# Kernel tuning notes

Measured on AMD Instinct MI355X. Metric: run time of the kernel, lower is better.

## Reference

```python
import jax, jax.numpy as jnp
import numpy as np

DIM = 96          # dense volume side (N_VOX / 2**(n_layer-scale-1) with scale=2)
C = 24            # ch_in[scale]
FEAT_INIT = 0.0   # not direct_substitute


def _scatter_channel(coords, values, ch, default, dtype=jnp.float32):
    """sparse_to_dense_channel: dense[x,y,z] = values; OOB coords are dropped."""
    vol = jnp.full((DIM, DIM, DIM, ch), default, dtype=dtype)
    return vol.at[coords[:, 0], coords[:, 1], coords[:, 2]].set(values, mode='drop')


def _mask_coords(coords, valid):
    # Replace invalid rows with an out-of-bounds index so scatter mode='drop' skips them
    return jnp.where(valid[:, None], coords, DIM)


def setup_inputs() -> dict:
    key = jax.random.key(0)
    ks = jax.random.split(key, 9)
    return {
        'current_coords': jax.random.randint(ks[0], (150000, 3), 0, DIM, dtype=jnp.int32),
        'current_values': jax.random.normal(ks[1], (150000, C), dtype=jnp.float32),
        'global_coords_raw': jax.random.randint(ks[2], (200000, 3), 0, 160, dtype=jnp.int32),
        'global_values': jax.random.normal(ks[3], (200000, C), dtype=jnp.float32),
        'coords_target_global': jax.random.randint(ks[4], (100000, 3), 0, DIM, dtype=jnp.int32),
        'tsdf_target': jax.random.uniform(ks[5], (100000,), dtype=jnp.float32) * 2.0 - 1.0,
        'global_coords_target_raw': jax.random.randint(ks[6], (120000, 3), 0, 160, dtype=jnp.int32),
        'global_tsdf_target': jax.random.uniform(ks[7], (120000, 1), dtype=jnp.float32) * 2.0 - 1.0,
        'relative_origin': jax.random.randint(ks[8], (3,), 0, 32, dtype=jnp.int32),
    }


def reference(current_coords, current_values, global_coords_raw, global_values,
              coords_target_global, tsdf_target, global_coords_target_raw,
              global_tsdf_target, relative_origin):
    # --- shift global coords into current fragment frame, compute FBV mask ---
    gc = global_coords_raw - relative_origin[None, :]
    valid = jnp.all((gc >= 0) & (gc < DIM), axis=-1)                     # (M,)

    # --- FUSION.FULL is False: keep only global voxels present in current sparse set ---
    valid_volume = jnp.zeros((DIM, DIM, DIM), dtype=jnp.int32)
    valid_volume = valid_volume.at[current_coords[:, 0], current_coords[:, 1],
                                   current_coords[:, 2]].set(1, mode='drop')
    gcc = jnp.clip(gc, 0, DIM - 1)
    occ = valid_volume[gcc[:, 0], gcc[:, 1], gcc[:, 2]]
    valid = valid & (occ != 0)

    # --- dense scatters (sparse_to_dense_channel) ---
    global_volume = _scatter_channel(_mask_coords(gc, valid), global_values, C, FEAT_INIT)
    current_volume = _scatter_channel(current_coords, current_values, C, FEAT_INIT)

    # updated_coords = current_coords (FULL is False branch)
    updated_coords = current_coords

    gtc = global_coords_target_raw - relative_origin[None, :]
    valid_target = jnp.all((gtc >= 0) & (gtc < DIM), axis=-1)            # (Mt,)
    coords_target = jnp.concatenate([_mask_coords(gtc, valid_target), coords_target_global], axis=0)
    tsdf_all = jnp.concatenate([global_tsdf_target, tsdf_target[:, None]], axis=0)
    target_volume = _scatter_channel(coords_target, tsdf_all, 1, 1.0)

    return updated_coords, current_volume, global_volume, target_volume, valid, valid_target
```

## Files before the change

### kernel.cpp

```cpp
#include <hip/hip_runtime.h>

#define DIMV 96
#define NCH 24
constexpr int VOX = DIMV * DIMV * DIMV;
constexpr int N_CUR = 150000;
constexpr int N_GLB = 200000;
constexpr int N_TGT_LOC = 100000;
constexpr int N_TGT_GLB = 120000;

constexpr size_t OFF_COORDS = 0;
constexpr size_t OFF_CURVOL = 450000;
constexpr size_t OFF_GLBVOL = OFF_CURVOL + (size_t)VOX * NCH;
constexpr size_t OFF_TGTVOL = OFF_GLBVOL + (size_t)VOX * NCH;
constexpr size_t OFF_VALID  = OFF_TGTVOL + (size_t)VOX;
constexpr size_t OFF_VALIDT = OFF_VALID + N_GLB;

typedef float v4f __attribute__((ext_vector_type(4)));
typedef int   v4i __attribute__((ext_vector_type(4)));

constexpr int N_COORD4 = (N_CUR * 3) / 4;
constexpr int NV4_WS   = (3 * VOX) / 4;

__device__ __forceinline__ int voxel_of(int x, int y, int z) {
    return (x * DIMV + y) * DIMV + z;
}

__global__ void __launch_bounds__(256) k_init(int* __restrict__ ws,
                                              const int* __restrict__ cur_coords,
                                              float* __restrict__ coords_out) {
    int i = blockIdx.x * blockDim.x + threadIdx.x;
    if (i < NV4_WS) {
        v4i m = {-1, -1, -1, -1};
        *((v4i*)ws + i) = m;
    } else if (i < NV4_WS + N_COORD4) {
        int j = i - NV4_WS;
        v4i c = *(const v4i*)(cur_coords + 4 * j);
        v4f f = {(float)c.x, (float)c.y, (float)c.z, (float)c.w};
        *((v4f*)coords_out + j) = f;
    }
}

__global__ void k_points(const int* __restrict__ cur_coords,
                         const int* __restrict__ tgt_coords_g,
                         const int* __restrict__ tgt_coords_l,
                         const int* __restrict__ glb_coords,
                         const int* __restrict__ origin,
                         int* __restrict__ w_cur,
                         int* __restrict__ w_tgt,
                         int* __restrict__ w_glb,
                         float* __restrict__ validt_out) {
    int i = blockIdx.x * blockDim.x + threadIdx.x;
    if (i < N_CUR) {
        int x = cur_coords[3 * i], y = cur_coords[3 * i + 1], z = cur_coords[3 * i + 2];
        if ((unsigned)x < DIMV && (unsigned)y < DIMV && (unsigned)z < DIMV)
            atomicMax(&w_cur[voxel_of(x, y, z)], i);
    } else if (i < N_CUR + N_TGT_GLB) {
        int j = i - N_CUR;
        int x = tgt_coords_g[3 * j]     - origin[0];
        int y = tgt_coords_g[3 * j + 1] - origin[1];
        int z = tgt_coords_g[3 * j + 2] - origin[2];
        bool inb = (unsigned)x < DIMV && (unsigned)y < DIMV && (unsigned)z < DIMV;
        validt_out[j] = inb ? 1.0f : 0.0f;
        if (inb) atomicMax(&w_tgt[voxel_of(x, y, z)], j);
    } else if (i < N_CUR + N_TGT_GLB + N_TGT_LOC) {
        int j = i - N_CUR - N_TGT_GLB;
        int x = tgt_coords_l[3 * j], y = tgt_coords_l[3 * j + 1], z = tgt_coords_l[3 * j + 2];
        if ((unsigned)x < DIMV && (unsigned)y < DIMV && (unsigned)z < DIMV)
            atomicMax(&w_tgt[voxel_of(x, y, z)], j + N_TGT_GLB);
    } else if (i < N_CUR + N_TGT_GLB + N_TGT_LOC + N_GLB) {
        int j = i - N_CUR - N_TGT_GLB - N_TGT_LOC;
        int x = glb_coords[3 * j]     - origin[0];
        int y = glb_coords[3 * j + 1] - origin[1];
        int z = glb_coords[3 * j + 2] - origin[2];
        if ((unsigned)x < DIMV && (unsigned)y < DIMV && (unsigned)z < DIMV)
            atomicMax(&w_glb[voxel_of(x, y, z)], j);
    }
}

__global__ void __launch_bounds__(256) k_fill_all(
                           const int* __restrict__ w_cur,
                           const int* __restrict__ w_glb,
                           const int* __restrict__ w_tgt,
                           const int* __restrict__ glb_coords,
                           const int* __restrict__ origin,
                           const float* __restrict__ cur_values,
                           const float* __restrict__ glb_values,
                           const float* __restrict__ glb_tsdf,
                           const float* __restrict__ loc_tsdf,
                           float* __restrict__ cur_out,
                           float* __restrict__ glb_out,
                           float* __restrict__ tgt_out,
                           float* __restrict__ valid_out) {
    int idx = blockIdx.x * blockDim.x + threadIdx.x;
    if (idx < N_GLB) {
        int x = glb_coords[3 * idx]     - origin[0];
        int y = glb_coords[3 * idx + 1] - origin[1];
        int z = glb_coords[3 * idx + 2] - origin[2];
        bool inb = (unsigned)x < DIMV && (unsigned)y < DIMV && (unsigned)z < DIMV;
        int cx = min(max(x, 0), DIMV - 1);
        int cy = min(max(y, 0), DIMV - 1);
        int cz = min(max(z, 0), DIMV - 1);
        bool valid = inb && (w_cur[voxel_of(cx, cy, cz)] >= 0);
        valid_out[idx] = valid ? 1.0f : 0.0f;
        return;
    }
    idx -= N_GLB;
    if (idx >= VOX * 6) return;
    int v = idx / 6, q = idx - v * 6;

    int wc = w_cur[v];
    v4f cval = (v4f){0.f, 0.f, 0.f, 0.f};
    if (wc >= 0) cval = *(const v4f*)(cur_values + (size_t)wc * NCH + q * 4);
    __builtin_nontemporal_store(cval, (v4f*)(cur_out + (size_t)v * NCH + q * 4));

    int wg = w_glb[v];
    v4f gval = (v4f){0.f, 0.f, 0.f, 0.f};
    if (wg >= 0 && wc >= 0)
        gval = *(const v4f*)(glb_values + (size_t)wg * NCH + q * 4);
    __builtin_nontemporal_store(gval, (v4f*)(glb_out + (size_t)v * NCH + q * 4));

    if (q == 0) {
        int wt = w_tgt[v];
        float tval = 1.0f;
        if (wt >= 0) tval = (wt < N_TGT_GLB) ? glb_tsdf[wt] : loc_tsdf[wt - N_TGT_GLB];
        __builtin_nontemporal_store(tval, tgt_out + v);
    }
}

extern "C" void kernel_launch(void* const* d_in, const int* in_sizes, int n_in,
                              void* d_out, int out_size, void* d_ws, size_t ws_size,
                              hipStream_t stream) {
    const int*   cur_coords   = (const int*)d_in[0];
    const float* cur_values   = (const float*)d_in[1];
    const int*   glb_coords   = (const int*)d_in[2];
    const float* glb_values   = (const float*)d_in[3];
    const int*   tgt_coords_l = (const int*)d_in[4];
    const float* tgt_tsdf_l   = (const float*)d_in[5];
    const int*   tgt_coords_g = (const int*)d_in[6];
    const float* tgt_tsdf_g   = (const float*)d_in[7];
    const int*   rel_origin   = (const int*)d_in[8];

    float* out = (float*)d_out;
    int* w_cur = (int*)d_ws;
    int* w_glb = w_cur + VOX;
    int* w_tgt = w_glb + VOX;

    const int T = 256;
    auto blocks = [](int n) { return (n + 255) / 256; };

    k_init<<<blocks(NV4_WS + N_COORD4), T, 0, stream>>>(
        (int*)d_ws, cur_coords, out + OFF_COORDS);

    k_points<<<blocks(N_CUR + N_TGT_GLB + N_TGT_LOC + N_GLB), T, 0, stream>>>(
        cur_coords, tgt_coords_g, tgt_coords_l, glb_coords, rel_origin,
        w_cur, w_tgt, w_glb, out + OFF_VALIDT);

    k_fill_all<<<blocks(N_GLB + VOX * 6), T, 0, stream>>>(
        w_cur, w_glb, w_tgt, glb_coords, rel_origin,
        cur_values, glb_values, tgt_tsdf_g, tgt_tsdf_l,
        out + OFF_CURVOL, out + OFF_GLBVOL, out + OFF_TGTVOL, out + OFF_VALID);
}
```

Measured before the change: 57.96 us.

## Memset dense volumes and scatter only winning points instead of gathering per voxel

The per-voxel gather fill is replaced. The dense output volumes are now zero or one filled with hipMemsetD32Async, and a point-parallel kernel then writes only the values of points that won the atomicMax for their voxel. The workspace init kernel becomes a memset, and the coordinate float conversion is folded into k_points. Bulk memset should stream at near peak bandwidth and the gathers from indirection tables shrink to the occupied voxels. In exchange there are more launches and the scattered writes are random.

```diff
diff --git a/kernel.cpp b/kernel.cpp
--- a/kernel.cpp
+++ b/kernel.cpp
@@ -19,25 +19,9 @@
 typedef int   v4i __attribute__((ext_vector_type(4)));
 
 constexpr int N_COORD4 = (N_CUR * 3) / 4;
-constexpr int NV4_WS   = (3 * VOX) / 4;
 
 __device__ __forceinline__ int voxel_of(int x, int y, int z) {
     return (x * DIMV + y) * DIMV + z;
-}
-
-__global__ void __launch_bounds__(256) k_init(int* __restrict__ ws,
-                                              const int* __restrict__ cur_coords,
-                                              float* __restrict__ coords_out) {
-    int i = blockIdx.x * blockDim.x + threadIdx.x;
-    if (i < NV4_WS) {
-        v4i m = {-1, -1, -1, -1};
-        *((v4i*)ws + i) = m;
-    } else if (i < NV4_WS + N_COORD4) {
-        int j = i - NV4_WS;
-        v4i c = *(const v4i*)(cur_coords + 4 * j);
-        v4f f = {(float)c.x, (float)c.y, (float)c.z, (float)c.w};
-        *((v4f*)coords_out + j) = f;
-    }
 }
 
 __global__ void k_points(const int* __restrict__ cur_coords,
@@ -48,7 +32,8 @@
                          int* __restrict__ w_cur,
                          int* __restrict__ w_tgt,
                          int* __restrict__ w_glb,
-                         float* __restrict__ validt_out) {
+                         float* __restrict__ validt_out,
+                         float* __restrict__ coords_out) {
     int i = blockIdx.x * blockDim.x + threadIdx.x;
     if (i < N_CUR) {
         int x = cur_coords[3 * i], y = cur_coords[3 * i + 1], z = cur_coords[3 * i + 2];
@@ -74,14 +59,26 @@
         int z = glb_coords[3 * j + 2] - origin[2];
         if ((unsigned)x < DIMV && (unsigned)y < DIMV && (unsigned)z < DIMV)
             atomicMax(&w_glb[voxel_of(x, y, z)], j);
+    } else if (i < N_CUR + N_TGT_GLB + N_TGT_LOC + N_GLB + N_COORD4) {
+        int j = i - N_CUR - N_TGT_GLB - N_TGT_LOC - N_GLB;
+        v4i c = *(const v4i*)(cur_coords + 4 * j);
+        v4f f = {(float)c.x, (float)c.y, (float)c.z, (float)c.w};
+        *((v4f*)coords_out + j) = f;
     }
 }
 
-__global__ void __launch_bounds__(256) k_fill_all(
+constexpr int SEG_A = N_CUR * 6;
+constexpr int SEG_B = N_GLB * 6;
+constexpr int SEG_C = N_TGT_GLB + N_TGT_LOC;
+
+__global__ void __launch_bounds__(256) k_payload(
                            const int* __restrict__ w_cur,
                            const int* __restrict__ w_glb,
                            const int* __restrict__ w_tgt,
+                           const int* __restrict__ cur_coords,
                            const int* __restrict__ glb_coords,
+                           const int* __restrict__ tgt_coords_g,
+                           const int* __restrict__ tgt_coords_l,
                            const int* __restrict__ origin,
                            const float* __restrict__ cur_values,
                            const float* __restrict__ glb_values,
@@ -91,39 +88,50 @@
                            float* __restrict__ glb_out,
                            float* __restrict__ tgt_out,
                            float* __restrict__ valid_out) {
-    int idx = blockIdx.x * blockDim.x + threadIdx.x;
-    if (idx < N_GLB) {
-        int x = glb_coords[3 * idx]     - origin[0];
-        int y = glb_coords[3 * idx + 1] - origin[1];
-        int z = glb_coords[3 * idx + 2] - origin[2];
+    int i = blockIdx.x * blockDim.x + threadIdx.x;
+    if (i < SEG_A) {
+        int p = i / 6, q = i - p * 6;
+        int x = cur_coords[3 * p], y = cur_coords[3 * p + 1], z = cur_coords[3 * p + 2];
+        if ((unsigned)x < DIMV && (unsigned)y < DIMV && (unsigned)z < DIMV) {
+            int v = voxel_of(x, y, z);
+            if (w_cur[v] == p)
+                *(v4f*)(cur_out + (size_t)v * NCH + q * 4) =
+                    *(const v4f*)(cur_values + (size_t)p * NCH + q * 4);
+        }
+    } else if (i < SEG_A + SEG_B) {
+        int t = i - SEG_A;
+        int p = t / 6, q = t - p * 6;
+        int x = glb_coords[3 * p]     - origin[0];
+        int y = glb_coords[3 * p + 1] - origin[1];
+        int z = glb_coords[3 * p + 2] - origin[2];
         bool inb = (unsigned)x < DIMV && (unsigned)y < DIMV && (unsigned)z < DIMV;
         int cx = min(max(x, 0), DIMV - 1);
         int cy = min(max(y, 0), DIMV - 1);
         int cz = min(max(z, 0), DIMV - 1);
-        bool valid = inb && (w_cur[voxel_of(cx, cy, cz)] >= 0);
-        valid_out[idx] = valid ? 1.0f : 0.0f;
-        return;
-    }
-    idx -= N_GLB;
-    if (idx >= VOX * 6) return;
-    int v = idx / 6, q = idx - v * 6;
-
-    int wc = w_cur[v];
-    v4f cval = (v4f){0.f, 0.f, 0.f, 0.f};
-    if (wc >= 0) cval = *(const v4f*)(cur_values + (size_t)wc * NCH + q * 4);
-    __builtin_nontemporal_store(cval, (v4f*)(cur_out + (size_t)v * NCH + q * 4));
-
-    int wg = w_glb[v];
-    v4f gval = (v4f){0.f, 0.f, 0.f, 0.f};
-    if (wg >= 0 && wc >= 0)
-        gval = *(const v4f*)(glb_values + (size_t)wg * NCH + q * 4);
-    __builtin_nontemporal_store(gval, (v4f*)(glb_out + (size_t)v * NCH + q * 4));
-
-    if (q == 0) {
-        int wt = w_tgt[v];
-        float tval = 1.0f;
-        if (wt >= 0) tval = (wt < N_TGT_GLB) ? glb_tsdf[wt] : loc_tsdf[wt - N_TGT_GLB];
-        __builtin_nontemporal_store(tval, tgt_out + v);
+        int v = voxel_of(cx, cy, cz);
+        bool occ = w_cur[v] >= 0;
+        if (q == 0) valid_out[p] = (inb && occ) ? 1.0f : 0.0f;
+        if (inb && occ && w_glb[v] == p)
+            *(v4f*)(glb_out + (size_t)v * NCH + q * 4) =
+                *(const v4f*)(glb_values + (size_t)p * NCH + q * 4);
+    } else if (i < SEG_A + SEG_B + SEG_C) {
+        int j = i - SEG_A - SEG_B;
+        if (j < N_TGT_GLB) {
+            int x = tgt_coords_g[3 * j]     - origin[0];
+            int y = tgt_coords_g[3 * j + 1] - origin[1];
+            int z = tgt_coords_g[3 * j + 2] - origin[2];
+            if ((unsigned)x < DIMV && (unsigned)y < DIMV && (unsigned)z < DIMV) {
+                int v = voxel_of(x, y, z);
+                if (w_tgt[v] == j) tgt_out[v] = glb_tsdf[j];
+            }
+        } else {
+            int jj = j - N_TGT_GLB;
+            int x = tgt_coords_l[3 * jj], y = tgt_coords_l[3 * jj + 1], z = tgt_coords_l[3 * jj + 2];
+            if ((unsigned)x < DIMV && (unsigned)y < DIMV && (unsigned)z < DIMV) {
+                int v = voxel_of(x, y, z);
+                if (w_tgt[v] == j) tgt_out[v] = loc_tsdf[jj];
+            }
+        }
     }
 }
 
@@ -148,15 +156,19 @@
     const int T = 256;
     auto blocks = [](int n) { return (n + 255) / 256; };
 
-    k_init<<<blocks(NV4_WS + N_COORD4), T, 0, stream>>>(
-        (int*)d_ws, cur_coords, out + OFF_COORDS);
+    (void)hipMemsetD32Async((hipDeviceptr_t)d_ws, (int)0xFFFFFFFF, (size_t)3 * VOX, stream);
 
-    k_points<<<blocks(N_CUR + N_TGT_GLB + N_TGT_LOC + N_GLB), T, 0, stream>>>(
+    k_points<<<blocks(N_CUR + N_TGT_GLB + N_TGT_LOC + N_GLB + N_COORD4), T, 0, stream>>>(
         cur_coords, tgt_coords_g, tgt_coords_l, glb_coords, rel_origin,
-        w_cur, w_tgt, w_glb, out + OFF_VALIDT);
+        w_cur, w_tgt, w_glb, out + OFF_VALIDT, out + OFF_COORDS);
 
-    k_fill_all<<<blocks(N_GLB + VOX * 6), T, 0, stream>>>(
-        w_cur, w_glb, w_tgt, glb_coords, rel_origin,
-        cur_values, glb_values, tgt_tsdf_g, tgt_tsdf_l,
+    (void)hipMemsetD32Async((hipDeviceptr_t)(out + OFF_CURVOL), 0,
+                            OFF_TGTVOL - OFF_CURVOL, stream);
+    (void)hipMemsetD32Async((hipDeviceptr_t)(out + OFF_TGTVOL), 0x3f800000,
+                            (size_t)VOX, stream);
+
+    k_payload<<<blocks(SEG_A + SEG_B + SEG_C), T, 0, stream>>>(
+        w_cur, w_glb, w_tgt, cur_coords, glb_coords, tgt_coords_g, tgt_coords_l,
+        rel_origin, cur_values, glb_values, tgt_tsdf_g, tgt_tsdf_l,
         out + OFF_CURVOL, out + OFF_GLBVOL, out + OFF_TGTVOL, out + OFF_VALID);
 }
```

After: 66.97 us. 1.16x slower.
